# Performance work log

Measured on AMD Instinct MI355X. Metric: run time of the kernel, lower is better.

Reference implementation:

```python
import jax, jax.numpy as jnp
import numpy as np

L = 8          # number of QTT cores = log2(init_reso)
RESO = 256     # init_reso
MAX_RANK = 256
N_SAMPLES = 4096


def _qtt_ranks(L, max_rank):
    return [min(8 ** k, 8 ** (L - k), max_rank) for k in range(L + 1)]


def setup_inputs() -> dict:
    key = jax.random.key(0)
    ranks = _qtt_ranks(L, MAX_RANK)
    keys = jax.random.split(key, L + 1)
    inp = {}
    for l in range(L):
        shape = (ranks[l], 8, ranks[l + 1])
        scale = (shape[0] * shape[1]) ** -0.5  # keep chain products O(1)
        inp[f"core{l}"] = jax.random.normal(keys[l], shape, dtype=jnp.float32) * scale
    inp["coords_xyz"] = jax.random.randint(keys[L], (N_SAMPLES, 3), 0, RESO)
    return inp


def _coords_to_qtt(coords_xyz, num_cores):
    # coords_xyz: (N, 3) int. Per core l (most-significant bit first):
    # c_l = 4*bit_x + 2*bit_y + bit_z in [0, 8)  -> shape (L, N)
    x, y, z = coords_xyz[:, 0], coords_xyz[:, 1], coords_xyz[:, 2]
    shifts = jnp.arange(num_cores - 1, -1, -1)[:, None]  # (L, 1)
    bx = (x[None, :] >> shifts) & 1
    by = (y[None, :] >> shifts) & 1
    bz = (z[None, :] >> shifts) & 1
    return 4 * bx + 2 * by + bz


def _sample_tt(cores, coords):
    # cores[l]: (r_l, 8, r_{l+1}); coords: (L, N)
    # v starts as first core slice: (N, r_1)  (r_0 == 1)
    v = cores[0][0, coords[0], :]
    for l in range(1, len(cores)):
        # gathered slice: (r_l, N, r_{l+1}) -> (N, r_l, r_{l+1})
        g = jnp.transpose(cores[l][:, coords[l], :], (1, 0, 2))
        v = jnp.einsum('nr,nrs->ns', v, g)
    return v[:, 0]  # r_L == 1 -> (N,)


def reference(core0, core1, core2, core3, core4, core5, core6, core7, coords_xyz):
    cores = [core0, core1, core2, core3, core4, core5, core6, core7]
    coords = _coords_to_qtt(coords_xyz, len(cores))
    return _sample_tt(cores, coords)
```

## Files before the change

### kernel.cpp

```cpp
#include <hip/hip_runtime.h>


typedef unsigned int u32;

__device__ __forceinline__ void async_load16(const float* g, float* l) {
    __builtin_amdgcn_global_load_lds(
        (const __attribute__((address_space(1))) u32*)g,
        (__attribute__((address_space(3))) u32*)l, 16, 0, 0);
}
__device__ __forceinline__ void fma4(float4& c, float a, const float4& b) {
    c.x = fmaf(a, b.x, c.x); c.y = fmaf(a, b.y, c.y);
    c.z = fmaf(a, b.z, c.z); c.w = fmaf(a, b.w, c.w);
}
__device__ __forceinline__ int digit_of(int x, int y, int z, int sh) {
    return 4*((x>>sh)&1) + 2*((y>>sh)&1) + ((z>>sh)&1);
}

__global__ __launch_bounds__(256, 3) void tables_kernel(
    const float* __restrict__ C0, const float* __restrict__ C1,
    const float* __restrict__ C2, const float* __restrict__ C3,
    const float* __restrict__ C5, const float* __restrict__ C6,
    const float* __restrict__ C7,
    const int* __restrict__ coords, int n,
    int* __restrict__ perms, int* __restrict__ bases,
    float* __restrict__ P3, float* __restrict__ T)
{
    __shared__ __align__(16) union {
        struct { unsigned char digs[8192]; int cnt[8]; int offs[8]; } p;
        struct { float S6s[8][64]; } b;
        struct { float v64[8][64]; float As[8][260]; float Bs[4][2][4][256]; } g;
    } u;
    const int t = threadIdx.x;
    const int ln = t & 63, wv = t >> 6;
    const int bx = blockIdx.x;

    if (bx == 0) {
        if (t < 8) u.p.cnt[t] = 0;
        __syncthreads();
        for (int i = t; i < n; i += 256) {
            const int d = digit_of(coords[3*i], coords[3*i+1], coords[3*i+2], 3);
            u.p.digs[i] = (unsigned char)d;
            atomicAdd(&u.p.cnt[d], 1);
        }
        __syncthreads();
        if (t == 0) {
            int run = 0;
            for (int d = 0; d < 8; ++d) {
                u.p.offs[d] = run;
                bases[d] = run;
                run += u.p.cnt[d];
            }
            bases[8] = run;
        }
        __syncthreads();
        for (int i = t; i < n; i += 256) {
            const int pos = atomicAdd(&u.p.offs[u.p.digs[i]], 1);
            perms[pos] = i;
        }
    } else if (bx < 65) {
        const int bb = bx - 1;
        const int d5 = bb >> 3, d6 = bb & 7;
#pragma unroll
        for (int j = 0; j < 2; ++j) {
            const int idx = t + 256*j, d7 = idx >> 6, s = idx & 63;
            float acc = 0.f;
#pragma unroll
            for (int jj = 0; jj < 8; ++jj)
                acc = fmaf(C6[s*64 + d6*8 + jj], C7[jj*8 + d7], acc);
            u.b.S6s[d7][s] = acc;
        }
        __syncthreads();
        float4 creg[16];
#pragma unroll
        for (int s4 = 0; s4 < 16; ++s4)
            creg[s4] = *(const float4*)(C5 + (size_t)t*512 + d5*64 + s4*4);
#pragma unroll 1
        for (int d7 = 0; d7 < 8; ++d7) {
            float acc = 0.f;
#pragma unroll
            for (int s4 = 0; s4 < 16; ++s4) {
                const float4 a = creg[s4];
                const float4 b = *(const float4*)&u.b.S6s[d7][s4*4];
                acc = fmaf(a.x, b.x, acc); acc = fmaf(a.y, b.y, acc);
                acc = fmaf(a.z, b.z, acc); acc = fmaf(a.w, b.w, acc);
            }
            T[(size_t)((d5*8 + d6)*8 + d7)*256 + t] = acc;
        }
    } else {
        const int bb = bx - 65;
        const int d3 = bb & 7, d2 = (bb >> 3) & 7, d0 = bb >> 6;
        const float* Cd = C3 + d3 * 256;
        float* BsF = &u.g.Bs[0][0][0][0];
        const int kbase = wv * 64;

#pragma unroll
        for (int j = 0; j < 4; ++j)
            async_load16(Cd + (size_t)(kbase + j)*2048 + ln*4,
                         &u.g.Bs[wv][0][j][ln*4]);

#pragma unroll
        for (int j = 0; j < 2; ++j) {
            const int idx = t + 256*j, d1 = idx >> 6, c = idx & 63;
            float acc = 0.f;
#pragma unroll
            for (int r = 0; r < 8; ++r)
                acc = fmaf(C0[d0*8 + r], C1[r*512 + d1*64 + c], acc);
            u.g.v64[d1][c] = acc;
        }
        __syncthreads();

        {
            float4 accA0 = make_float4(0,0,0,0), accA1 = make_float4(0,0,0,0);
#pragma unroll 8
            for (int j = 0; j < 64; ++j) {
                const float4 c2 = *(const float4*)(C2 + (size_t)j*2048 + d2*256 + ln*4);
                fma4(accA0, u.g.v64[wv*2 + 0][j], c2);
                fma4(accA1, u.g.v64[wv*2 + 1][j], c2);
            }
            *(float4*)&u.g.As[wv*2 + 0][ln*4] = accA0;
            *(float4*)&u.g.As[wv*2 + 1][ln*4] = accA1;
        }
        __syncthreads();

        float4 acc[8];
#pragma unroll
        for (int r = 0; r < 8; ++r) acc[r] = make_float4(0,0,0,0);

#pragma unroll 1
        for (int s = 0; s < 16; ++s) {
            if (s < 15) {
                const int nb = (s + 1) & 1;
                const int ko = kbase + (s + 1) * 4;
#pragma unroll
                for (int j = 0; j < 4; ++j)
                    async_load16(Cd + (size_t)(ko + j)*2048 + ln*4,
                                 &u.g.Bs[wv][nb][j][ln*4]);
                asm volatile("s_waitcnt vmcnt(4)" ::: "memory");
            } else {
                asm volatile("s_waitcnt vmcnt(0)" ::: "memory");
            }
            __builtin_amdgcn_sched_barrier(0);
            const int cb = s & 1, kb = kbase + s * 4;
            const float4 b0v = *(const float4*)&u.g.Bs[wv][cb][0][ln*4];
            const float4 b1v = *(const float4*)&u.g.Bs[wv][cb][1][ln*4];
            const float4 b2v = *(const float4*)&u.g.Bs[wv][cb][2][ln*4];
            const float4 b3v = *(const float4*)&u.g.Bs[wv][cb][3][ln*4];
#pragma unroll
            for (int r = 0; r < 8; ++r) {
                const float4 a = *(const float4*)&u.g.As[r][kb];
                fma4(acc[r], a.x, b0v); fma4(acc[r], a.y, b1v);
                fma4(acc[r], a.z, b2v); fma4(acc[r], a.w, b3v);
            }
        }

        {
            float* my = BsF + wv * 2048;
#pragma unroll
            for (int r = 0; r < 8; ++r)
                *(float4*)&my[r*256 + ln*4] = acc[r];
        }
        __syncthreads();
#pragma unroll
        for (int i = 0; i < 2; ++i) {
            const int r = wv*2 + i;
            float4 v = *(const float4*)&BsF[       r*256 + ln*4];
            const float4 p1 = *(const float4*)&BsF[2048 + r*256 + ln*4];
            const float4 p2 = *(const float4*)&BsF[4096 + r*256 + ln*4];
            const float4 p3 = *(const float4*)&BsF[6144 + r*256 + ln*4];
            v.x += p1.x + p2.x + p3.x; v.y += p1.y + p2.y + p3.y;
            v.z += p1.z + p2.z + p3.z; v.w += p1.w + p2.w + p3.w;
            const int ai = d0*512 + r*64 + d2*8 + d3;
            *(float4*)(P3 + (size_t)ai*256 + ln*4) = v;
        }
    }
}

__global__ __launch_bounds__(256, 2) void stage4_final_kernel(
    const float* __restrict__ P3, const float* __restrict__ C4,
    const float* __restrict__ T, const int* __restrict__ coords,
    const int* __restrict__ perm, const int* __restrict__ base,
    float* __restrict__ out)
{
    const int d = blockIdx.x;
    const int b0 = base[d], b1 = base[d + 1];
    const int nrows = b1 - b0;
    const int t = threadIdx.x, ln = t & 63, wv = t >> 6;

    __shared__ __align__(16) float Arm[8][260];
    __shared__ __align__(16) float Bs[4][2][4][256];
    __shared__ int rows[8], aidx[8], qs[8];
    float* BsF = &Bs[0][0][0][0];

    const float* Cd = C4 + d * 256;
    const int kbase = wv * 64;

    for (int tile = blockIdx.y; tile * 8 < nrows; tile += (int)gridDim.y) {
        const int row0 = b0 + tile * 8;

#pragma unroll
        for (int j = 0; j < 4; ++j)
            async_load16(Cd + (size_t)(kbase + j)*2048 + ln*4,
                         &Bs[wv][0][j][ln*4]);

        if (t < 8) {
            const int gr = row0 + t;
            const int rr = (gr < b1) ? perm[gr] : -1;
            rows[t] = rr;
            int a = 0, q = 0;
            if (rr >= 0) {
                const int x = coords[3*rr], y = coords[3*rr+1], z = coords[3*rr+2];
                a = digit_of(x,y,z,7)*512 + digit_of(x,y,z,6)*64
                  + digit_of(x,y,z,5)*8 + digit_of(x,y,z,4);
                q = digit_of(x,y,z,2)*64 + digit_of(x,y,z,1)*8 + digit_of(x,y,z,0);
            }
            aidx[t] = a; qs[t] = q;
        }
        __syncthreads();

#pragma unroll
        for (int j = 0; j < 2; ++j) {
            const int idx = t + 256*j, s = idx >> 6, c4 = idx & 63;
            float4 v = make_float4(0,0,0,0);
            if (rows[s] >= 0)
                v = *(const float4*)(P3 + (size_t)aidx[s]*256 + c4*4);
            *(float4*)&Arm[s][c4*4] = v;
        }
        __syncthreads();

        float4 acc[8];
#pragma unroll
        for (int r = 0; r < 8; ++r) acc[r] = make_float4(0,0,0,0);

#pragma unroll 1
        for (int s = 0; s < 16; ++s) {
            if (s < 15) {
                const int nb = (s + 1) & 1;
                const int ko = kbase + (s + 1) * 4;
#pragma unroll
                for (int j = 0; j < 4; ++j)
                    async_load16(Cd + (size_t)(ko + j)*2048 + ln*4,
                                 &Bs[wv][nb][j][ln*4]);
                asm volatile("s_waitcnt vmcnt(4)" ::: "memory");
            } else {
                asm volatile("s_waitcnt vmcnt(0)" ::: "memory");
            }
            __builtin_amdgcn_sched_barrier(0);
            const int cb = s & 1, kb = kbase + s * 4;
            const float4 b0v = *(const float4*)&Bs[wv][cb][0][ln*4];
            const float4 b1v = *(const float4*)&Bs[wv][cb][1][ln*4];
            const float4 b2v = *(const float4*)&Bs[wv][cb][2][ln*4];
            const float4 b3v = *(const float4*)&Bs[wv][cb][3][ln*4];
#pragma unroll
            for (int r = 0; r < 8; ++r) {
                const float4 a = *(const float4*)&Arm[r][kb];
                fma4(acc[r], a.x, b0v); fma4(acc[r], a.y, b1v);
                fma4(acc[r], a.z, b2v); fma4(acc[r], a.w, b3v);
            }
        }

        {
            float* my = BsF + wv * 2048;
#pragma unroll
            for (int r = 0; r < 8; ++r)
                *(float4*)&my[r*256 + ln*4] = acc[r];
        }
        __syncthreads();

#pragma unroll
        for (int i = 0; i < 2; ++i) {
            const int r = wv*2 + i;
            const int rr = rows[r];
            float p = 0.f;
            if (rr >= 0) {
                float4 v = *(const float4*)&BsF[       r*256 + ln*4];
                const float4 p1 = *(const float4*)&BsF[2048 + r*256 + ln*4];
                const float4 p2 = *(const float4*)&BsF[4096 + r*256 + ln*4];
                const float4 p3 = *(const float4*)&BsF[6144 + r*256 + ln*4];
                v.x += p1.x + p2.x + p3.x; v.y += p1.y + p2.y + p3.y;
                v.z += p1.z + p2.z + p3.z; v.w += p1.w + p2.w + p3.w;
                const float4 tv = *(const float4*)(T + (size_t)qs[r]*256 + ln*4);
                p = fmaf(v.x, tv.x, fmaf(v.y, tv.y, fmaf(v.z, tv.z, v.w * tv.w)));
            }
            p += __shfl_xor(p, 1);
            p += __shfl_xor(p, 2);
            p += __shfl_xor(p, 4);
            p += __shfl_xor(p, 8);
            p += __shfl_xor(p, 16);
            p += __shfl_xor(p, 32);
            if (ln == 0 && rr >= 0) out[rr] = p;
        }
        __syncthreads();
    }
}

extern "C" void kernel_launch(void* const* d_in, const int* in_sizes, int n_in,
                              void* d_out, int out_size, void* d_ws, size_t ws_size,
                              hipStream_t stream) {
    const float* C0 = (const float*)d_in[0];
    const float* C1 = (const float*)d_in[1];
    const float* C2 = (const float*)d_in[2];
    const float* C3 = (const float*)d_in[3];
    const float* C4 = (const float*)d_in[4];
    const float* C5 = (const float*)d_in[5];
    const float* C6 = (const float*)d_in[6];
    const float* C7 = (const float*)d_in[7];
    const int* coords = (const int*)d_in[8];
    float* out = (float*)d_out;

    const int n = in_sizes[8] / 3;

    float* P3   = (float*)d_ws;
    float* Tt   = P3 + 4096*256;
    int*   perms = (int*)(Tt + 512*256);
    int*   bases = perms + (size_t)n;

    tables_kernel<<<577, 256, 0, stream>>>(
        C0, C1, C2, C3, C5, C6, C7, coords, n, perms, bases, P3, Tt);
    stage4_final_kernel<<<dim3(8, 64), 256, 0, stream>>>(
        P3, C4, Tt, coords, perms, bases, out);
}
```

Measured before the change: 115.3 us.

## Precompute right-side table U via C4 contraction, replace sorted stage4 with per-sample dot

Instead of sorting samples by the middle digit and running a per-sample GEMM against core4, the right half is contracted into a dense table U (all 4096 d4,q combinations × 256) using a transposed C4. P3 is computed in the same launch as U. A final kernel then does one 256-length dot product per sample. This removes the permutation/sort pass and the sample-dependent GEMM, at the cost of an extra prep launch, a C4 transpose and a full 4096×256 GEMM for U regardless of how many samples there are.

```diff
diff --git a/kernel.cpp b/kernel.cpp
--- a/kernel.cpp
+++ b/kernel.cpp
@@ -16,50 +16,76 @@
     return 4*((x>>sh)&1) + 2*((y>>sh)&1) + ((z>>sh)&1);
 }
 
-__global__ __launch_bounds__(256, 3) void tables_kernel(
-    const float* __restrict__ C0, const float* __restrict__ C1,
-    const float* __restrict__ C2, const float* __restrict__ C3,
-    const float* __restrict__ C5, const float* __restrict__ C6,
-    const float* __restrict__ C7,
-    const int* __restrict__ coords, int n,
-    int* __restrict__ perms, int* __restrict__ bases,
-    float* __restrict__ P3, float* __restrict__ T)
-{
-    __shared__ __align__(16) union {
-        struct { unsigned char digs[8192]; int cnt[8]; int offs[8]; } p;
-        struct { float S6s[8][64]; } b;
-        struct { float v64[8][64]; float As[8][260]; float Bs[4][2][4][256]; } g;
-    } u;
+__device__ __forceinline__ void kgemm_reduce_store(
+    const float* __restrict__ Cd, int rowStride,
+    const float (*As)[260], float* BsF,
+    float* __restrict__ outP, int rowBase, int rowStep,
+    int ln, int wv)
+{
+    const int kbase = wv * 64;
+    float4 acc[8];
+#pragma unroll
+    for (int r = 0; r < 8; ++r) acc[r] = make_float4(0,0,0,0);
+
+#pragma unroll 1
+    for (int s = 0; s < 16; ++s) {
+        if (s < 15) {
+            const int nb = (s + 1) & 1;
+            const int ko = kbase + (s + 1) * 4;
+#pragma unroll
+            for (int j = 0; j < 4; ++j)
+                async_load16(Cd + (size_t)(ko + j)*rowStride + ln*4,
+                             BsF + wv*2048 + nb*1024 + j*256 + ln*4);
+            asm volatile("s_waitcnt vmcnt(4)" ::: "memory");
+        } else {
+            asm volatile("s_waitcnt vmcnt(0)" ::: "memory");
+        }
+        __builtin_amdgcn_sched_barrier(0);
+        const int cb = s & 1, kb = kbase + s * 4;
+        const float* Bp = BsF + wv*2048 + cb*1024;
+        const float4 b0v = *(const float4*)(Bp +   0 + ln*4);
+        const float4 b1v = *(const float4*)(Bp + 256 + ln*4);
+        const float4 b2v = *(const float4*)(Bp + 512 + ln*4);
+        const float4 b3v = *(const float4*)(Bp + 768 + ln*4);
+#pragma unroll
+        for (int r = 0; r < 8; ++r) {
+            const float4 a = *(const float4*)&As[r][kb];
+            fma4(acc[r], a.x, b0v); fma4(acc[r], a.y, b1v);
+            fma4(acc[r], a.z, b2v); fma4(acc[r], a.w, b3v);
+        }
+    }
+
+    {
+        float* my = BsF + wv * 2048;
+#pragma unroll
+        for (int r = 0; r < 8; ++r)
+            *(float4*)(my + r*256 + ln*4) = acc[r];
+    }
+    __syncthreads();
+#pragma unroll
+    for (int i = 0; i < 2; ++i) {
+        const int r = wv*2 + i;
+        float4 v        = *(const float4*)(BsF +        r*256 + ln*4);
+        const float4 p1 = *(const float4*)(BsF + 2048 + r*256 + ln*4);
+        const float4 p2 = *(const float4*)(BsF + 4096 + r*256 + ln*4);
+        const float4 p3 = *(const float4*)(BsF + 6144 + r*256 + ln*4);
+        v.x += p1.x + p2.x + p3.x; v.y += p1.y + p2.y + p3.y;
+        v.z += p1.z + p2.z + p3.z; v.w += p1.w + p2.w + p3.w;
+        *(float4*)(outP + (size_t)(rowBase + r*rowStep)*256 + ln*4) = v;
+    }
+}
+
+__global__ __launch_bounds__(256, 4) void prep_kernel(
+    const float* __restrict__ C4, const float* __restrict__ C5,
+    const float* __restrict__ C6, const float* __restrict__ C7,
+    float* __restrict__ T, float* __restrict__ C4t)
+{
     const int t = threadIdx.x;
-    const int ln = t & 63, wv = t >> 6;
     const int bx = blockIdx.x;
 
-    if (bx == 0) {
-        if (t < 8) u.p.cnt[t] = 0;
-        __syncthreads();
-        for (int i = t; i < n; i += 256) {
-            const int d = digit_of(coords[3*i], coords[3*i+1], coords[3*i+2], 3);
-            u.p.digs[i] = (unsigned char)d;
-            atomicAdd(&u.p.cnt[d], 1);
-        }
-        __syncthreads();
-        if (t == 0) {
-            int run = 0;
-            for (int d = 0; d < 8; ++d) {
-                u.p.offs[d] = run;
-                bases[d] = run;
-                run += u.p.cnt[d];
-            }
-            bases[8] = run;
-        }
-        __syncthreads();
-        for (int i = t; i < n; i += 256) {
-            const int pos = atomicAdd(&u.p.offs[u.p.digs[i]], 1);
-            perms[pos] = i;
-        }
-    } else if (bx < 65) {
-        const int bb = bx - 1;
-        const int d5 = bb >> 3, d6 = bb & 7;
+    if (bx < 64) {
+        __shared__ float S6s[8][64];
+        const int d5 = bx >> 3, d6 = bx & 7;
 #pragma unroll
         for (int j = 0; j < 2; ++j) {
             const int idx = t + 256*j, d7 = idx >> 6, s = idx & 63;
@@ -67,7 +93,7 @@
 #pragma unroll
             for (int jj = 0; jj < 8; ++jj)
                 acc = fmaf(C6[s*64 + d6*8 + jj], C7[jj*8 + d7], acc);
-            u.b.S6s[d7][s] = acc;
+            S6s[d7][s] = acc;
         }
         __syncthreads();
         float4 creg[16];
@@ -80,23 +106,47 @@
 #pragma unroll
             for (int s4 = 0; s4 < 16; ++s4) {
                 const float4 a = creg[s4];
-                const float4 b = *(const float4*)&u.b.S6s[d7][s4*4];
+                const float4 b = *(const float4*)&S6s[d7][s4*4];
                 acc = fmaf(a.x, b.x, acc); acc = fmaf(a.y, b.y, acc);
                 acc = fmaf(a.z, b.z, acc); acc = fmaf(a.w, b.w, acc);
             }
             T[(size_t)((d5*8 + d6)*8 + d7)*256 + t] = acc;
         }
     } else {
-        const int bb = bx - 65;
-        const int d3 = bb & 7, d2 = (bb >> 3) & 7, d0 = bb >> 6;
+        const int cb = bx - 64;
+        const int d4 = cb >> 2, s5q = cb & 3;
+#pragma unroll 8
+        for (int j = 0; j < 64; ++j) {
+            const int s5 = s5q*64 + j;
+            C4t[(size_t)d4*65536 + (size_t)s5*256 + t] =
+                C4[(size_t)t*2048 + d4*256 + s5];
+        }
+    }
+}
+
+__global__ __launch_bounds__(256, 3) void tables_kernel(
+    const float* __restrict__ C0, const float* __restrict__ C1,
+    const float* __restrict__ C2, const float* __restrict__ C3,
+    const float* __restrict__ T, const float* __restrict__ C4t,
+    float* __restrict__ P3, float* __restrict__ U)
+{
+    __shared__ __align__(16) struct {
+        float v64[8][64]; float As[8][260]; float Bs[4][2][4][256];
+    } u;
+    const int t = threadIdx.x;
+    const int ln = t & 63, wv = t >> 6;
+    const int bx = blockIdx.x;
+    float* BsF = &u.Bs[0][0][0][0];
+    const int kbase = wv * 64;
+
+    if (bx < 512) {
+        const int d3 = bx & 7, d2 = (bx >> 3) & 7, d0 = bx >> 6;
         const float* Cd = C3 + d3 * 256;
-        float* BsF = &u.g.Bs[0][0][0][0];
-        const int kbase = wv * 64;
 
 #pragma unroll
         for (int j = 0; j < 4; ++j)
             async_load16(Cd + (size_t)(kbase + j)*2048 + ln*4,
-                         &u.g.Bs[wv][0][j][ln*4]);
+                         BsF + wv*2048 + j*256 + ln*4);
 
 #pragma unroll
         for (int j = 0; j < 2; ++j) {
@@ -105,7 +155,7 @@
 #pragma unroll
             for (int r = 0; r < 8; ++r)
                 acc = fmaf(C0[d0*8 + r], C1[r*512 + d1*64 + c], acc);
-            u.g.v64[d1][c] = acc;
+            u.v64[d1][c] = acc;
         }
         __syncthreads();
 
@@ -114,183 +164,60 @@
 #pragma unroll 8
             for (int j = 0; j < 64; ++j) {
                 const float4 c2 = *(const float4*)(C2 + (size_t)j*2048 + d2*256 + ln*4);
-                fma4(accA0, u.g.v64[wv*2 + 0][j], c2);
-                fma4(accA1, u.g.v64[wv*2 + 1][j], c2);
+                fma4(accA0, u.v64[wv*2 + 0][j], c2);
+                fma4(accA1, u.v64[wv*2 + 1][j], c2);
             }
-            *(float4*)&u.g.As[wv*2 + 0][ln*4] = accA0;
-            *(float4*)&u.g.As[wv*2 + 1][ln*4] = accA1;
-        }
-        __syncthreads();
-
-        float4 acc[8];
-#pragma unroll
-        for (int r = 0; r < 8; ++r) acc[r] = make_float4(0,0,0,0);
-
-#pragma unroll 1
-        for (int s = 0; s < 16; ++s) {
-            if (s < 15) {
-                const int nb = (s + 1) & 1;
-                const int ko = kbase + (s + 1) * 4;
-#pragma unroll
-                for (int j = 0; j < 4; ++j)
-                    async_load16(Cd + (size_t)(ko + j)*2048 + ln*4,
-                                 &u.g.Bs[wv][nb][j][ln*4]);
-                asm volatile("s_waitcnt vmcnt(4)" ::: "memory");
-            } else {
-                asm volatile("s_waitcnt vmcnt(0)" ::: "memory");
-            }
-            __builtin_amdgcn_sched_barrier(0);
-            const int cb = s & 1, kb = kbase + s * 4;
-            const float4 b0v = *(const float4*)&u.g.Bs[wv][cb][0][ln*4];
-            const float4 b1v = *(const float4*)&u.g.Bs[wv][cb][1][ln*4];
-            const float4 b2v = *(const float4*)&u.g.Bs[wv][cb][2][ln*4];
-            const float4 b3v = *(const float4*)&u.g.Bs[wv][cb][3][ln*4];
-#pragma unroll
-            for (int r = 0; r < 8; ++r) {
-                const float4 a = *(const float4*)&u.g.As[r][kb];
-                fma4(acc[r], a.x, b0v); fma4(acc[r], a.y, b1v);
-                fma4(acc[r], a.z, b2v); fma4(acc[r], a.w, b3v);
-            }
-        }
-
-        {
-            float* my = BsF + wv * 2048;
-#pragma unroll
-            for (int r = 0; r < 8; ++r)
-                *(float4*)&my[r*256 + ln*4] = acc[r];
-        }
-        __syncthreads();
+            *(float4*)&u.As[wv*2 + 0][ln*4] = accA0;
+            *(float4*)&u.As[wv*2 + 1][ln*4] = accA1;
+        }
+        __syncthreads();
+
+        kgemm_reduce_store(Cd, 2048, u.As, BsF,
+                           P3, d0*512 + d2*8 + d3, 64, ln, wv);
+    } else {
+        const int ub = bx - 512;
+        const int qtile = ub & 63, d4 = ub >> 6;
+        const float* Cd = C4t + (size_t)d4*65536;
+
+#pragma unroll
+        for (int j = 0; j < 4; ++j)
+            async_load16(Cd + (size_t)(kbase + j)*256 + ln*4,
+                         BsF + wv*2048 + j*256 + ln*4);
 #pragma unroll
         for (int i = 0; i < 2; ++i) {
             const int r = wv*2 + i;
-            float4 v = *(const float4*)&BsF[       r*256 + ln*4];
-            const float4 p1 = *(const float4*)&BsF[2048 + r*256 + ln*4];
-            const float4 p2 = *(const float4*)&BsF[4096 + r*256 + ln*4];
-            const float4 p3 = *(const float4*)&BsF[6144 + r*256 + ln*4];
-            v.x += p1.x + p2.x + p3.x; v.y += p1.y + p2.y + p3.y;
-            v.z += p1.z + p2.z + p3.z; v.w += p1.w + p2.w + p3.w;
-            const int ai = d0*512 + r*64 + d2*8 + d3;
-            *(float4*)(P3 + (size_t)ai*256 + ln*4) = v;
-        }
-    }
-}
-
-__global__ __launch_bounds__(256, 2) void stage4_final_kernel(
-    const float* __restrict__ P3, const float* __restrict__ C4,
-    const float* __restrict__ T, const int* __restrict__ coords,
-    const int* __restrict__ perm, const int* __restrict__ base,
-    float* __restrict__ out)
-{
-    const int d = blockIdx.x;
-    const int b0 = base[d], b1 = base[d + 1];
-    const int nrows = b1 - b0;
-    const int t = threadIdx.x, ln = t & 63, wv = t >> 6;
-
-    __shared__ __align__(16) float Arm[8][260];
-    __shared__ __align__(16) float Bs[4][2][4][256];
-    __shared__ int rows[8], aidx[8], qs[8];
-    float* BsF = &Bs[0][0][0][0];
-
-    const float* Cd = C4 + d * 256;
-    const int kbase = wv * 64;
-
-    for (int tile = blockIdx.y; tile * 8 < nrows; tile += (int)gridDim.y) {
-        const int row0 = b0 + tile * 8;
-
-#pragma unroll
-        for (int j = 0; j < 4; ++j)
-            async_load16(Cd + (size_t)(kbase + j)*2048 + ln*4,
-                         &Bs[wv][0][j][ln*4]);
-
-        if (t < 8) {
-            const int gr = row0 + t;
-            const int rr = (gr < b1) ? perm[gr] : -1;
-            rows[t] = rr;
-            int a = 0, q = 0;
-            if (rr >= 0) {
-                const int x = coords[3*rr], y = coords[3*rr+1], z = coords[3*rr+2];
-                a = digit_of(x,y,z,7)*512 + digit_of(x,y,z,6)*64
-                  + digit_of(x,y,z,5)*8 + digit_of(x,y,z,4);
-                q = digit_of(x,y,z,2)*64 + digit_of(x,y,z,1)*8 + digit_of(x,y,z,0);
-            }
-            aidx[t] = a; qs[t] = q;
-        }
-        __syncthreads();
-
-#pragma unroll
-        for (int j = 0; j < 2; ++j) {
-            const int idx = t + 256*j, s = idx >> 6, c4 = idx & 63;
-            float4 v = make_float4(0,0,0,0);
-            if (rows[s] >= 0)
-                v = *(const float4*)(P3 + (size_t)aidx[s]*256 + c4*4);
-            *(float4*)&Arm[s][c4*4] = v;
-        }
-        __syncthreads();
-
-        float4 acc[8];
-#pragma unroll
-        for (int r = 0; r < 8; ++r) acc[r] = make_float4(0,0,0,0);
-
-#pragma unroll 1
-        for (int s = 0; s < 16; ++s) {
-            if (s < 15) {
-                const int nb = (s + 1) & 1;
-                const int ko = kbase + (s + 1) * 4;
-#pragma unroll
-                for (int j = 0; j < 4; ++j)
-                    async_load16(Cd + (size_t)(ko + j)*2048 + ln*4,
-                                 &Bs[wv][nb][j][ln*4]);
-                asm volatile("s_waitcnt vmcnt(4)" ::: "memory");
-            } else {
-                asm volatile("s_waitcnt vmcnt(0)" ::: "memory");
-            }
-            __builtin_amdgcn_sched_barrier(0);
-            const int cb = s & 1, kb = kbase + s * 4;
-            const float4 b0v = *(const float4*)&Bs[wv][cb][0][ln*4];
-            const float4 b1v = *(const float4*)&Bs[wv][cb][1][ln*4];
-            const float4 b2v = *(const float4*)&Bs[wv][cb][2][ln*4];
-            const float4 b3v = *(const float4*)&Bs[wv][cb][3][ln*4];
-#pragma unroll
-            for (int r = 0; r < 8; ++r) {
-                const float4 a = *(const float4*)&Arm[r][kb];
-                fma4(acc[r], a.x, b0v); fma4(acc[r], a.y, b1v);
-                fma4(acc[r], a.z, b2v); fma4(acc[r], a.w, b3v);
-            }
-        }
-
-        {
-            float* my = BsF + wv * 2048;
-#pragma unroll
-            for (int r = 0; r < 8; ++r)
-                *(float4*)&my[r*256 + ln*4] = acc[r];
-        }
-        __syncthreads();
-
-#pragma unroll
-        for (int i = 0; i < 2; ++i) {
-            const int r = wv*2 + i;
-            const int rr = rows[r];
-            float p = 0.f;
-            if (rr >= 0) {
-                float4 v = *(const float4*)&BsF[       r*256 + ln*4];
-                const float4 p1 = *(const float4*)&BsF[2048 + r*256 + ln*4];
-                const float4 p2 = *(const float4*)&BsF[4096 + r*256 + ln*4];
-                const float4 p3 = *(const float4*)&BsF[6144 + r*256 + ln*4];
-                v.x += p1.x + p2.x + p3.x; v.y += p1.y + p2.y + p3.y;
-                v.z += p1.z + p2.z + p3.z; v.w += p1.w + p2.w + p3.w;
-                const float4 tv = *(const float4*)(T + (size_t)qs[r]*256 + ln*4);
-                p = fmaf(v.x, tv.x, fmaf(v.y, tv.y, fmaf(v.z, tv.z, v.w * tv.w)));
-            }
-            p += __shfl_xor(p, 1);
-            p += __shfl_xor(p, 2);
-            p += __shfl_xor(p, 4);
-            p += __shfl_xor(p, 8);
-            p += __shfl_xor(p, 16);
-            p += __shfl_xor(p, 32);
-            if (ln == 0 && rr >= 0) out[rr] = p;
-        }
-        __syncthreads();
-    }
+            async_load16(T + (size_t)(qtile*8 + r)*256 + ln*4, &u.As[r][ln*4]);
+        }
+        __syncthreads();
+
+        kgemm_reduce_store(Cd, 256, u.As, BsF,
+                           U, d4*512 + qtile*8, 1, ln, wv);
+    }
+}
+
+__global__ __launch_bounds__(256) void final_kernel(
+    const float* __restrict__ P3, const float* __restrict__ U,
+    const int* __restrict__ coords, int n, float* __restrict__ out)
+{
+    const int ln = threadIdx.x & 63, wv = threadIdx.x >> 6;
+    const int s = blockIdx.x * 4 + wv;
+    if (s >= n) return;
+    const int x = coords[3*s], y = coords[3*s+1], z = coords[3*s+2];
+    const int a  = digit_of(x,y,z,7)*512 + digit_of(x,y,z,6)*64
+                 + digit_of(x,y,z,5)*8  + digit_of(x,y,z,4);
+    const int d4 = digit_of(x,y,z,3);
+    const int q  = digit_of(x,y,z,2)*64 + digit_of(x,y,z,1)*8
+                 + digit_of(x,y,z,0);
+    const float4 p4 = *(const float4*)(P3 + (size_t)a*256 + ln*4);
+    const float4 u4 = *(const float4*)(U + (size_t)(d4*512 + q)*256 + ln*4);
+    float p = fmaf(p4.x, u4.x, fmaf(p4.y, u4.y, fmaf(p4.z, u4.z, p4.w*u4.w)));
+    p += __shfl_xor(p, 1);
+    p += __shfl_xor(p, 2);
+    p += __shfl_xor(p, 4);
+    p += __shfl_xor(p, 8);
+    p += __shfl_xor(p, 16);
+    p += __shfl_xor(p, 32);
+    if (ln == 0) out[s] = p;
 }
 
 extern "C" void kernel_launch(void* const* d_in, const int* in_sizes, int n_in,
@@ -309,13 +236,12 @@
 
     const int n = in_sizes[8] / 3;
 
-    float* P3   = (float*)d_ws;
-    float* Tt   = P3 + 4096*256;
-    int*   perms = (int*)(Tt + 512*256);
-    int*   bases = perms + (size_t)n;
-
-    tables_kernel<<<577, 256, 0, stream>>>(
-        C0, C1, C2, C3, C5, C6, C7, coords, n, perms, bases, P3, Tt);
-    stage4_final_kernel<<<dim3(8, 64), 256, 0, stream>>>(
-        P3, C4, Tt, coords, perms, bases, out);
-}
+    float* P3  = (float*)d_ws;
+    float* U   = P3  + 4096*256;
+    float* Tt  = U   + 4096*256;
+    float* C4t = Tt  + 512*256;
+
+    prep_kernel<<<96, 256, 0, stream>>>(C4, C5, C6, C7, Tt, C4t);
+    tables_kernel<<<1024, 256, 0, stream>>>(C0, C1, C2, C3, Tt, C4t, P3, U);
+    final_kernel<<<(n + 3) / 4, 256, 0, stream>>>(P3, U, coords, n, out);
+}
```

Result: slower. 118.7 us (+3.0%).

## Widen GEMM row tiles from 8 to 16 rows in both kernels

Applied to the files above, without the earlier changes.

Both the stage-3 table GEMM and the stage-4 gather GEMM now process 16 A-rows per block instead of 8. Each streamed B tile (C3/C4 slices) is reused across twice as many rows, which halves the B traffic and the number of blocks (321 and 8x32 grids). The cost is doubled accumulator registers (16 float4), two-phase reduction through shared memory, larger LDS use, and fewer blocks, which may reduce parallelism. Launch bounds for the stage-4 kernel change to 3.

```diff
diff --git a/kernel.cpp b/kernel.cpp
--- a/kernel.cpp
+++ b/kernel.cpp
@@ -14,6 +14,69 @@
 }
 __device__ __forceinline__ int digit_of(int x, int y, int z, int sh) {
     return 4*((x>>sh)&1) + 2*((y>>sh)&1) + ((z>>sh)&1);
+}
+
+__device__ __forceinline__ void kgemm16(
+    const float* __restrict__ Cd, int rowStride,
+    const float (*As)[260], float* BsF,
+    float* __restrict__ outP, int rowBase, int mulLo,
+    int ln, int wv)
+{
+    const int kbase = wv * 64;
+    float4 acc[16];
+#pragma unroll
+    for (int r = 0; r < 16; ++r) acc[r] = make_float4(0,0,0,0);
+
+#pragma unroll 1
+    for (int s = 0; s < 16; ++s) {
+        if (s < 15) {
+            const int nb = (s + 1) & 1;
+            const int ko = kbase + (s + 1) * 4;
+#pragma unroll
+            for (int j = 0; j < 4; ++j)
+                async_load16(Cd + (size_t)(ko + j)*rowStride + ln*4,
+                             BsF + wv*2048 + nb*1024 + j*256 + ln*4);
+            asm volatile("s_waitcnt vmcnt(4)" ::: "memory");
+        } else {
+            asm volatile("s_waitcnt vmcnt(0)" ::: "memory");
+        }
+        __builtin_amdgcn_sched_barrier(0);
+        const int cb = s & 1, kb = kbase + s * 4;
+        const float* Bp = BsF + wv*2048 + cb*1024;
+        const float4 b0v = *(const float4*)(Bp +   0 + ln*4);
+        const float4 b1v = *(const float4*)(Bp + 256 + ln*4);
+        const float4 b2v = *(const float4*)(Bp + 512 + ln*4);
+        const float4 b3v = *(const float4*)(Bp + 768 + ln*4);
+#pragma unroll
+        for (int r = 0; r < 16; ++r) {
+            const float4 a = *(const float4*)&As[r][kb];
+            fma4(acc[r], a.x, b0v); fma4(acc[r], a.y, b1v);
+            fma4(acc[r], a.z, b2v); fma4(acc[r], a.w, b3v);
+        }
+    }
+
+#pragma unroll
+    for (int ph = 0; ph < 2; ++ph) {
+        float* my = BsF + wv * 2048;
+#pragma unroll
+        for (int r8 = 0; r8 < 8; ++r8)
+            *(float4*)(my + r8*256 + ln*4) = acc[ph*8 + r8];
+        __syncthreads();
+#pragma unroll
+        for (int i = 0; i < 2; ++i) {
+            const int rr = wv*2 + i;
+            float4 v        = *(const float4*)(BsF +        rr*256 + ln*4);
+            const float4 p1 = *(const float4*)(BsF + 2048 + rr*256 + ln*4);
+            const float4 p2 = *(const float4*)(BsF + 4096 + rr*256 + ln*4);
+            const float4 p3 = *(const float4*)(BsF + 6144 + rr*256 + ln*4);
+            v.x += p1.x + p2.x + p3.x; v.y += p1.y + p2.y + p3.y;
+            v.z += p1.z + p2.z + p3.z; v.w += p1.w + p2.w + p3.w;
+            const int r = ph*8 + rr;
+            const int row = rowBase + mulLo*(r & 7) + 8*(r >> 3);
+            *(float4*)(outP + (size_t)row*256 + ln*4) = v;
+        }
+        __syncthreads();
+    }
 }
 
 __global__ __launch_bounds__(256, 3) void tables_kernel(
@@ -28,7 +91,7 @@
     __shared__ __align__(16) union {
         struct { unsigned char digs[8192]; int cnt[8]; int offs[8]; } p;
         struct { float S6s[8][64]; } b;
-        struct { float v64[8][64]; float As[8][260]; float Bs[4][2][4][256]; } g;
+        struct { float v64[8][64]; float As[16][260]; float Bs[4][2][4][256]; } g;
     } u;
     const int t = threadIdx.x;
     const int ln = t & 63, wv = t >> 6;
@@ -88,7 +151,7 @@
         }
     } else {
         const int bb = bx - 65;
-        const int d3 = bb & 7, d2 = (bb >> 3) & 7, d0 = bb >> 6;
+        const int d3 = bb & 7, d2p = (bb >> 3) & 3, d0 = bb >> 5;
         const float* Cd = C3 + d3 * 256;
         float* BsF = &u.g.Bs[0][0][0][0];
         const int kbase = wv * 64;
@@ -96,7 +159,7 @@
 #pragma unroll
         for (int j = 0; j < 4; ++j)
             async_load16(Cd + (size_t)(kbase + j)*2048 + ln*4,
-                         &u.g.Bs[wv][0][j][ln*4]);
+                         BsF + wv*2048 + j*256 + ln*4);
 
 #pragma unroll
         for (int j = 0; j < 2; ++j) {
@@ -110,72 +173,30 @@
         __syncthreads();
 
         {
-            float4 accA0 = make_float4(0,0,0,0), accA1 = make_float4(0,0,0,0);
+            const int rbase = wv * 4;
+            const int d2 = d2p*2 + (rbase >> 3);
+            float4 a0 = make_float4(0,0,0,0), a1 = make_float4(0,0,0,0);
+            float4 a2 = make_float4(0,0,0,0), a3 = make_float4(0,0,0,0);
 #pragma unroll 8
             for (int j = 0; j < 64; ++j) {
                 const float4 c2 = *(const float4*)(C2 + (size_t)j*2048 + d2*256 + ln*4);
-                fma4(accA0, u.g.v64[wv*2 + 0][j], c2);
-                fma4(accA1, u.g.v64[wv*2 + 1][j], c2);
-            }
-            *(float4*)&u.g.As[wv*2 + 0][ln*4] = accA0;
-            *(float4*)&u.g.As[wv*2 + 1][ln*4] = accA1;
-        }
-        __syncthreads();
-
-        float4 acc[8];
-#pragma unroll
-        for (int r = 0; r < 8; ++r) acc[r] = make_float4(0,0,0,0);
-
-#pragma unroll 1
-        for (int s = 0; s < 16; ++s) {
-            if (s < 15) {
-                const int nb = (s + 1) & 1;
-                const int ko = kbase + (s + 1) * 4;
-#pragma unroll
-                for (int j = 0; j < 4; ++j)
-                    async_load16(Cd + (size_t)(ko + j)*2048 + ln*4,
-                                 &u.g.Bs[wv][nb][j][ln*4]);
-                asm volatile("s_waitcnt vmcnt(4)" ::: "memory");
-            } else {
-                asm volatile("s_waitcnt vmcnt(0)" ::: "memory");
-            }
-            __builtin_amdgcn_sched_barrier(0);
-            const int cb = s & 1, kb = kbase + s * 4;
-            const float4 b0v = *(const float4*)&u.g.Bs[wv][cb][0][ln*4];
-            const float4 b1v = *(const float4*)&u.g.Bs[wv][cb][1][ln*4];
-            const float4 b2v = *(const float4*)&u.g.Bs[wv][cb][2][ln*4];
-            const float4 b3v = *(const float4*)&u.g.Bs[wv][cb][3][ln*4];
-#pragma unroll
-            for (int r = 0; r < 8; ++r) {
-                const float4 a = *(const float4*)&u.g.As[r][kb];
-                fma4(acc[r], a.x, b0v); fma4(acc[r], a.y, b1v);
-                fma4(acc[r], a.z, b2v); fma4(acc[r], a.w, b3v);
-            }
-        }
-
-        {
-            float* my = BsF + wv * 2048;
-#pragma unroll
-            for (int r = 0; r < 8; ++r)
-                *(float4*)&my[r*256 + ln*4] = acc[r];
-        }
-        __syncthreads();
-#pragma unroll
-        for (int i = 0; i < 2; ++i) {
-            const int r = wv*2 + i;
-            float4 v = *(const float4*)&BsF[       r*256 + ln*4];
-            const float4 p1 = *(const float4*)&BsF[2048 + r*256 + ln*4];
-            const float4 p2 = *(const float4*)&BsF[4096 + r*256 + ln*4];
-            const float4 p3 = *(const float4*)&BsF[6144 + r*256 + ln*4];
-            v.x += p1.x + p2.x + p3.x; v.y += p1.y + p2.y + p3.y;
-            v.z += p1.z + p2.z + p3.z; v.w += p1.w + p2.w + p3.w;
-            const int ai = d0*512 + r*64 + d2*8 + d3;
-            *(float4*)(P3 + (size_t)ai*256 + ln*4) = v;
-        }
+                fma4(a0, u.g.v64[(rbase+0)&7][j], c2);
+                fma4(a1, u.g.v64[(rbase+1)&7][j], c2);
+                fma4(a2, u.g.v64[(rbase+2)&7][j], c2);
+                fma4(a3, u.g.v64[(rbase+3)&7][j], c2);
+            }
+            *(float4*)&u.g.As[rbase+0][ln*4] = a0;
+            *(float4*)&u.g.As[rbase+1][ln*4] = a1;
+            *(float4*)&u.g.As[rbase+2][ln*4] = a2;
+            *(float4*)&u.g.As[rbase+3][ln*4] = a3;
+        }
+        __syncthreads();
+
+        kgemm16(Cd, 2048, u.g.As, BsF, P3, d0*512 + d2p*16 + d3, 64, ln, wv);
     }
 }
 
-__global__ __launch_bounds__(256, 2) void stage4_final_kernel(
+__global__ __launch_bounds__(256, 3) void stage4_final_kernel(
     const float* __restrict__ P3, const float* __restrict__ C4,
     const float* __restrict__ T, const int* __restrict__ coords,
     const int* __restrict__ perm, const int* __restrict__ base,
@@ -186,23 +207,23 @@
     const int nrows = b1 - b0;
     const int t = threadIdx.x, ln = t & 63, wv = t >> 6;
 
-    __shared__ __align__(16) float Arm[8][260];
+    __shared__ __align__(16) float As[16][260];
     __shared__ __align__(16) float Bs[4][2][4][256];
-    __shared__ int rows[8], aidx[8], qs[8];
+    __shared__ int rows[16], aidx[16], qs[16];
     float* BsF = &Bs[0][0][0][0];
 
     const float* Cd = C4 + d * 256;
     const int kbase = wv * 64;
 
-    for (int tile = blockIdx.y; tile * 8 < nrows; tile += (int)gridDim.y) {
-        const int row0 = b0 + tile * 8;
+    for (int tile = blockIdx.y; tile * 16 < nrows; tile += (int)gridDim.y) {
+        const int row0 = b0 + tile * 16;
 
 #pragma unroll
         for (int j = 0; j < 4; ++j)
             async_load16(Cd + (size_t)(kbase + j)*2048 + ln*4,
-                         &Bs[wv][0][j][ln*4]);
-
-        if (t < 8) {
+                         BsF + wv*2048 + j*256 + ln*4);
+
+        if (t < 16) {
             const int gr = row0 + t;
             const int rr = (gr < b1) ? perm[gr] : -1;
             rows[t] = rr;
@@ -218,18 +239,18 @@
         __syncthreads();
 
 #pragma unroll
-        for (int j = 0; j < 2; ++j) {
+        for (int j = 0; j < 4; ++j) {
             const int idx = t + 256*j, s = idx >> 6, c4 = idx & 63;
             float4 v = make_float4(0,0,0,0);
             if (rows[s] >= 0)
                 v = *(const float4*)(P3 + (size_t)aidx[s]*256 + c4*4);
-            *(float4*)&Arm[s][c4*4] = v;
-        }
-        __syncthreads();
-
-        float4 acc[8];
-#pragma unroll
-        for (int r = 0; r < 8; ++r) acc[r] = make_float4(0,0,0,0);
+            *(float4*)&As[s][c4*4] = v;
+        }
+        __syncthreads();
+
+        float4 acc[16];
+#pragma unroll
+        for (int r = 0; r < 16; ++r) acc[r] = make_float4(0,0,0,0);
 
 #pragma unroll 1
         for (int s = 0; s < 16; ++s) {
@@ -239,57 +260,60 @@
 #pragma unroll
                 for (int j = 0; j < 4; ++j)
                     async_load16(Cd + (size_t)(ko + j)*2048 + ln*4,
-                                 &Bs[wv][nb][j][ln*4]);
+                                 BsF + wv*2048 + nb*1024 + j*256 + ln*4);
                 asm volatile("s_waitcnt vmcnt(4)" ::: "memory");
             } else {
                 asm volatile("s_waitcnt vmcnt(0)" ::: "memory");
             }
             __builtin_amdgcn_sched_barrier(0);
             const int cb = s & 1, kb = kbase + s * 4;
-            const float4 b0v = *(const float4*)&Bs[wv][cb][0][ln*4];
-            const float4 b1v = *(const float4*)&Bs[wv][cb][1][ln*4];
-            const float4 b2v = *(const float4*)&Bs[wv][cb][2][ln*4];
-            const float4 b3v = *(const float4*)&Bs[wv][cb][3][ln*4];
-#pragma unroll
-            for (int r = 0; r < 8; ++r) {
-                const float4 a = *(const float4*)&Arm[r][kb];
+            const float* Bp = BsF + wv*2048 + cb*1024;
+            const float4 b0v = *(const float4*)(Bp +   0 + ln*4);
+            const float4 b1v = *(const float4*)(Bp + 256 + ln*4);
+            const float4 b2v = *(const float4*)(Bp + 512 + ln*4);
+            const float4 b3v = *(const float4*)(Bp + 768 + ln*4);
+#pragma unroll
+            for (int r = 0; r < 16; ++r) {
+                const float4 a = *(const float4*)&As[r][kb];
                 fma4(acc[r], a.x, b0v); fma4(acc[r], a.y, b1v);
                 fma4(acc[r], a.z, b2v); fma4(acc[r], a.w, b3v);
             }
         }
 
-        {
+#pragma unroll
+        for (int ph = 0; ph < 2; ++ph) {
             float* my = BsF + wv * 2048;
 #pragma unroll
-            for (int r = 0; r < 8; ++r)
-                *(float4*)&my[r*256 + ln*4] = acc[r];
-        }
-        __syncthreads();
-
-#pragma unroll
-        for (int i = 0; i < 2; ++i) {
-            const int r = wv*2 + i;
-            const int rr = rows[r];
-            float p = 0.f;
-            if (rr >= 0) {
-                float4 v = *(const float4*)&BsF[       r*256 + ln*4];
-                const float4 p1 = *(const float4*)&BsF[2048 + r*256 + ln*4];
-                const float4 p2 = *(const float4*)&BsF[4096 + r*256 + ln*4];
-                const float4 p3 = *(const float4*)&BsF[6144 + r*256 + ln*4];
-                v.x += p1.x + p2.x + p3.x; v.y += p1.y + p2.y + p3.y;
-                v.z += p1.z + p2.z + p3.z; v.w += p1.w + p2.w + p3.w;
-                const float4 tv = *(const float4*)(T + (size_t)qs[r]*256 + ln*4);
-                p = fmaf(v.x, tv.x, fmaf(v.y, tv.y, fmaf(v.z, tv.z, v.w * tv.w)));
-            }
-            p += __shfl_xor(p, 1);
-            p += __shfl_xor(p, 2);
-            p += __shfl_xor(p, 4);
-            p += __shfl_xor(p, 8);
-            p += __shfl_xor(p, 16);
-            p += __shfl_xor(p, 32);
-            if (ln == 0 && rr >= 0) out[rr] = p;
-        }
-        __syncthreads();
+            for (int r8 = 0; r8 < 8; ++r8)
+                *(float4*)(my + r8*256 + ln*4) = acc[ph*8 + r8];
+            __syncthreads();
+#pragma unroll
+            for (int i = 0; i < 2; ++i) {
+                const int rr8 = wv*2 + i;
+                const int sIdx = ph*8 + rr8;
+                const int rr = rows[sIdx];
+                float p = 0.f;
+                if (rr >= 0) {
+                    float4 v        = *(const float4*)(BsF +        rr8*256 + ln*4);
+                    const float4 p1 = *(const float4*)(BsF + 2048 + rr8*256 + ln*4);
+                    const float4 p2 = *(const float4*)(BsF + 4096 + rr8*256 + ln*4);
+                    const float4 p3 = *(const float4*)(BsF + 6144 + rr8*256 + ln*4);
+                    v.x += p1.x + p2.x + p3.x; v.y += p1.y + p2.y + p3.y;
+                    v.z += p1.z + p2.z + p3.z; v.w += p1.w + p2.w + p3.w;
+                    const float4 tv = *(const float4*)(T + (size_t)qs[sIdx]*256 + ln*4);
+                    p = fmaf(v.x, tv.x, fmaf(v.y, tv.y,
+                        fmaf(v.z, tv.z, v.w * tv.w)));
+                }
+                p += __shfl_xor(p, 1);
+                p += __shfl_xor(p, 2);
+                p += __shfl_xor(p, 4);
+                p += __shfl_xor(p, 8);
+                p += __shfl_xor(p, 16);
+                p += __shfl_xor(p, 32);
+                if (ln == 0 && rr >= 0) out[rr] = p;
+            }
+            __syncthreads();
+        }
     }
 }
 
@@ -314,8 +338,8 @@
     int*   perms = (int*)(Tt + 512*256);
     int*   bases = perms + (size_t)n;
 
-    tables_kernel<<<577, 256, 0, stream>>>(
+    tables_kernel<<<321, 256, 0, stream>>>(
         C0, C1, C2, C3, C5, C6, C7, coords, n, perms, bases, P3, Tt);
-    stage4_final_kernel<<<dim3(8, 64), 256, 0, stream>>>(
+    stage4_final_kernel<<<dim3(8, 32), 256, 0, stream>>>(
         P3, C4, Tt, coords, perms, bases, out);
 }
```

New measurement: 121.7 us. 5.6% more time.
